# Performance work log

Hardware: AMD Instinct MI355X
Metric: run time of the kernel (lower is better)

Reference implementation:

```python
import jax, jax.numpy as jnp
import numpy as np

B, C, H, W = 64, 32, 112, 112
RANK = 3


def setup_inputs() -> dict:
    key = jax.random.key(0)
    k1, k2, k3, k4, k5 = jax.random.split(key, 5)
    N = H * W  # 12544
    return {
        "x": jax.random.uniform(k1, (B, C, H, W), dtype=jnp.float32),
        "p_buffer": jax.random.normal(k2, (B, N, RANK), dtype=jnp.float32),
        "q_buffer": jax.random.normal(k3, (B, C, RANK), dtype=jnp.float32),
        "grad_p_buffer": jax.random.normal(k4, (B, N, RANK), dtype=jnp.float32),
        "grad_q_buffer": jax.random.normal(k5, (B, C, RANK), dtype=jnp.float32),
        "n_iter": 2,
    }


def _power_svd(X, P, Q, n_iter):
    # X: [b, c, n]; P: [b, n, r]; Q: [b, c, r]
    for i in range(n_iter):
        if i == n_iter - 1:
            P = jnp.linalg.qr(P)[0]  # batched reduced QR, tall-skinny (n x r)
        Q = jnp.einsum('bcn,bnr->bcr', X, P)
        if i == n_iter - 1:
            Q = jnp.linalg.qr(Q)[0]  # batched reduced QR (c x r)
        P = jnp.einsum('bcn,bcr->bnr', X, Q)  # X^T @ Q
    return P, Q


def reference(x, p_buffer, q_buffer, grad_p_buffer, grad_q_buffer, n_iter):
    shape = x.shape
    X = x.reshape(shape[0], shape[1], -1)  # [B, C, H*W]
    P, Q = _power_svd(X, p_buffer, q_buffer, n_iter)
    # low-rank reconstruction Q @ P^T, back to original shape
    return jnp.einsum('bcr,bnr->bcn', Q, P).reshape(shape)
```

## Files before the change

### kernel.cpp

```cpp
#include <hip/hip_runtime.h>
#include <math.h>

#define N_HW 12544
#define TN 128
#define NCH 98
#define KB 16

#define WS_QG 65536
#define WS_U  (WS_QG + 64*96)
#define ZTOT  (WS_U)

typedef __attribute__((ext_vector_type(8)))  short short8;
typedef __attribute__((ext_vector_type(16))) float f32x16;
typedef __attribute__((ext_vector_type(4)))  float f32x4;

#define MFMA(a, b, c) __builtin_amdgcn_mfma_f32_32x32x16_bf16((a), (b), (c), 0, 0, 0)

__device__ __forceinline__ void split3(float f, ushort& h, ushort& m, ushort& l) {
    unsigned u = __builtin_bit_cast(unsigned, f);
    h = (ushort)(u >> 16);
    float fh = __builtin_bit_cast(float, u & 0xffff0000u);
    float rm = f - fh;
    unsigned um = __builtin_bit_cast(unsigned, rm);
    m = (ushort)(um >> 16);
    float fm = __builtin_bit_cast(float, um & 0xffff0000u);
    float rl = rm - fm;
    l = (ushort)(__builtin_bit_cast(unsigned, rl) >> 16);
}

__device__ __forceinline__ int xq(int c, int o) {
    return c * 16 + ((o & 8) | ((o ^ c) & 7));
}

__global__ __launch_bounds__(256)
void k0_zero(float* __restrict__ ws)
{
    const int g = blockIdx.x * 256 + threadIdx.x;
    if (g < ZTOT / 4) ((float4*)ws)[g] = make_float4(0.f, 0.f, 0.f, 0.f);
}

__global__ __launch_bounds__(256)
void k1_gram(const float* __restrict__ x, const float* __restrict__ p,
             float* __restrict__ Sg, float* __restrict__ Qg)
{
    const int b = blockIdx.y, kb = blockIdx.x;
    const int tid = threadIdx.x;
    const int lane = tid & 63, wave = tid >> 6;

    __shared__ uint4 XS[3 * 512];
    __shared__ alignas(16) ushort PTH[3 * TN], PTM[3 * TN], PTL[3 * TN];
    __shared__ float Ssum[1024], T2[1024], T3[1024];
    float* dmp = (float*)XS;

    const int c = tid >> 3, oc = tid & 7;
    const float* xrow = x + ((size_t)b * 32 + c) * N_HW;
    const float* pbat = p + (size_t)b * N_HW * 3;

    f32x16 D1 = {0,0,0,0,0,0,0,0,0,0,0,0,0,0,0,0};
    f32x16 D2 = {0,0,0,0,0,0,0,0,0,0,0,0,0,0,0,0};
    f32x16 D3 = {0,0,0,0,0,0,0,0,0,0,0,0,0,0,0,0};
    f32x16 DQ = {0,0,0,0,0,0,0,0,0,0,0,0,0,0,0,0};
    const int cl = lane & 31, g = lane >> 5;
    const int rr = (cl < 3) ? cl : 0;

    float4 pre[4];
    float prep[3];
    int j = kb;
    {
        const float4* xr = (const float4*)(xrow + (size_t)j * TN);
        pre[0] = xr[2 * oc];      pre[1] = xr[2 * oc + 1];
        pre[2] = xr[2 * oc + 16]; pre[3] = xr[2 * oc + 17];
        if (tid < TN) {
            const float* pb = pbat + (size_t)(j * TN + tid) * 3;
            prep[0] = pb[0]; prep[1] = pb[1]; prep[2] = pb[2];
        }
    }

    while (true) {
        #pragma unroll
        for (int t = 0; t < 2; ++t) {
            const int o = oc + 8 * t;
            float4 f0 = pre[2 * t], f1 = pre[2 * t + 1];
            float fv[8] = {f0.x, f0.y, f0.z, f0.w, f1.x, f1.y, f1.z, f1.w};
            unsigned hw[4], mw[4], lw[4];
            #pragma unroll
            for (int i = 0; i < 4; ++i) {
                ushort h0, m0, l0, h1, m1, l1;
                split3(fv[2 * i],     h0, m0, l0);
                split3(fv[2 * i + 1], h1, m1, l1);
                hw[i] = (unsigned)h0 | ((unsigned)h1 << 16);
                mw[i] = (unsigned)m0 | ((unsigned)m1 << 16);
                lw[i] = (unsigned)l0 | ((unsigned)l1 << 16);
            }
            const int s = xq(c, o);
            XS[s]        = make_uint4(hw[0], hw[1], hw[2], hw[3]);
            XS[512 + s]  = make_uint4(mw[0], mw[1], mw[2], mw[3]);
            XS[1024 + s] = make_uint4(lw[0], lw[1], lw[2], lw[3]);
        }
        if (tid < TN) {
            #pragma unroll
            for (int r = 0; r < 3; ++r) {
                ushort h, m, l;
                split3(prep[r], h, m, l);
                PTH[r * TN + tid] = h; PTM[r * TN + tid] = m; PTL[r * TN + tid] = l;
            }
        }

        const int jn = j + KB;
        const bool more = (jn < NCH);
        if (more) {
            const float4* xr = (const float4*)(xrow + (size_t)jn * TN);
            pre[0] = xr[2 * oc];      pre[1] = xr[2 * oc + 1];
            pre[2] = xr[2 * oc + 16]; pre[3] = xr[2 * oc + 17];
            if (tid < TN) {
                const float* pb = pbat + (size_t)(jn * TN + tid) * 3;
                prep[0] = pb[0]; prep[1] = pb[1]; prep[2] = pb[2];
            }
        }
        __syncthreads();

        for (int s = wave; s < 8; s += 4) {
            const int sl = xq(cl, 2 * s + g);
            short8 xh = __builtin_bit_cast(short8, XS[sl]);
            short8 xm = __builtin_bit_cast(short8, XS[512 + sl]);
            short8 xl = __builtin_bit_cast(short8, XS[1024 + sl]);
            const int po = rr * TN + 16 * s + 8 * g;
            short8 ph = *(const short8*)&PTH[po];
            short8 pm = *(const short8*)&PTM[po];
            short8 pl = *(const short8*)&PTL[po];
            D1 = MFMA(xh, xh, D1);
            D1 = MFMA(xm, xm, D1);
            D2 = MFMA(xh, xm, D2);
            D3 = MFMA(xh, xl, D3);
            DQ = MFMA(xh, ph, DQ);
            DQ = MFMA(xh, pm, DQ);
            DQ = MFMA(xm, ph, DQ);
            DQ = MFMA(xh, pl, DQ);
            DQ = MFMA(xl, ph, DQ);
            DQ = MFMA(xm, pm, DQ);
        }

        if (!more) break;
        j = jn;
        __syncthreads();
    }

    #define DUMP_REDUCE(D, dst)                                                            \
        __syncthreads();                                                                   \
        _Pragma("unroll")                                                                  \
        for (int i = 0; i < 4; ++i)                                                        \
            *(float4*)&dmp[tid * 20 + 4 * i] =                                             \
                make_float4((D)[4*i], (D)[4*i+1], (D)[4*i+2], (D)[4*i+3]);                 \
        __syncthreads();                                                                   \
        _Pragma("unroll")                                                                  \
        for (int it = 0; it < 4; ++it) {                                                   \
            const int e = tid + 256 * it;                                                  \
            const int r = e >> 5, co = e & 31;                                             \
            const int ln = co + 32 * ((r >> 2) & 1);                                       \
            const int rg = (r & 3) + 4 * (r >> 3);                                         \
            (dst)[e] = dmp[ln * 20 + rg] + dmp[(64 + ln) * 20 + rg]                        \
                     + dmp[(128 + ln) * 20 + rg] + dmp[(192 + ln) * 20 + rg];              \
        }

    DUMP_REDUCE(D1, Ssum)
    DUMP_REDUCE(D2, T2)
    DUMP_REDUCE(D3, T3)
    __syncthreads();
    {
        float* Sb = Sg + (size_t)b * 1024;
        #pragma unroll
        for (int it = 0; it < 4; ++it) {
            const int e = tid + 256 * it;
            const int r = e >> 5, co = e & 31;
            const int et = (co << 5) | r;
            atomicAdd(&Sb[e], Ssum[e] + T2[e] + T2[et] + T3[e] + T3[et]);
        }
    }
    __syncthreads();
    #pragma unroll
    for (int i = 0; i < 4; ++i)
        *(float4*)&dmp[tid * 20 + 4 * i] = make_float4(DQ[4*i], DQ[4*i+1], DQ[4*i+2], DQ[4*i+3]);
    __syncthreads();
    if (tid < 96) {
        const int c2 = tid / 3, r2 = tid - 3 * c2;
        const int ln = r2 + 32 * ((c2 >> 2) & 1);
        const int rg = (c2 & 3) + 4 * (c2 >> 3);
        float s = dmp[ln * 20 + rg] + dmp[(64 + ln) * 20 + rg]
                + dmp[(128 + ln) * 20 + rg] + dmp[(192 + ln) * 20 + rg];
        atomicAdd(&Qg[(size_t)b * 96 + tid], s);
    }
}

__global__ __launch_bounds__(128)
void k2_solve(const float* __restrict__ Sg, const float* __restrict__ Qg,
              float* __restrict__ Uo)
{
    const int b = blockIdx.x, tid = threadIdx.x;
    __shared__ float S[1024];
    __shared__ float Qv[96];
    __shared__ float V[96];
    __shared__ float G[6], L[6];

    #pragma unroll
    for (int i = 0; i < 8; ++i) S[tid + 128 * i] = Sg[(size_t)b * 1024 + tid + 128 * i];
    if (tid < 96) Qv[tid] = Qg[(size_t)b * 96 + tid];
    __syncthreads();
    if (tid < 96) {
        const int c = tid / 3, r = tid % 3;
        float s = 0.f;
        #pragma unroll 8
        for (int cc = 0; cc < 32; ++cc) s += S[c * 32 + cc] * Qv[cc * 3 + r];
        V[tid] = s;
    }
    for (int round = 0; round < 2; ++round) {
        __syncthreads();
        if (tid < 6) {
            const int r = (tid > 2) ? 2 : ((tid > 0) ? 1 : 0);
            const int s = tid - (r * (r + 1)) / 2;
            float g = 0.f;
            for (int c = 0; c < 32; ++c) g += V[c * 3 + r] * V[c * 3 + s];
            G[tid] = g;
        }
        __syncthreads();
        if (tid == 0) {
            const float l00 = sqrtf(G[0]);
            const float l10 = G[1] / l00, l20 = G[3] / l00;
            const float l11 = sqrtf(G[2] - l10 * l10);
            const float l21 = (G[4] - l20 * l10) / l11;
            const float l22 = sqrtf(G[5] - l20 * l20 - l21 * l21);
            L[0] = l00; L[1] = l10; L[2] = l11; L[3] = l20; L[4] = l21; L[5] = l22;
        }
        __syncthreads();
        if (tid < 32) {
            const float v0 = V[tid * 3 + 0], v1 = V[tid * 3 + 1], v2 = V[tid * 3 + 2];
            const float u0 = v0 / L[0];
            const float u1 = (v1 - L[1] * u0) / L[2];
            const float u2 = (v2 - L[3] * u0 - L[4] * u1) / L[5];
            V[tid * 3 + 0] = u0; V[tid * 3 + 1] = u1; V[tid * 3 + 2] = u2;
        }
    }
    __syncthreads();
    if (tid < 32) {
        Uo[(size_t)b * 128 + tid * 4 + 0] = V[tid * 3 + 0];
        Uo[(size_t)b * 128 + tid * 4 + 1] = V[tid * 3 + 1];
        Uo[(size_t)b * 128 + tid * 4 + 2] = V[tid * 3 + 2];
        Uo[(size_t)b * 128 + tid * 4 + 3] = 0.f;
    }
}

__global__ __launch_bounds__(256)
void k3_out(const float* __restrict__ x, const float* __restrict__ Uw,
            float* __restrict__ out)
{
    const int b = blockIdx.y, tid = threadIdx.x;
    __shared__ float Us[32][4];
    if (tid < 128) ((float*)Us)[tid] = Uw[(size_t)b * 128 + tid];
    __syncthreads();
    const int g = blockIdx.x * 256 + tid;
    if (g >= N_HW / 4) return;

    const float* Xb = x   + (size_t)b * 32 * N_HW + 4 * (size_t)g;
    float*       Ob = out + (size_t)b * 32 * N_HW + 4 * (size_t)g;

    float t0x = 0, t0y = 0, t0z = 0, t0w = 0;
    float t1x = 0, t1y = 0, t1z = 0, t1w = 0;
    float t2x = 0, t2y = 0, t2z = 0, t2w = 0;
    #pragma unroll 16
    for (int c = 0; c < 32; ++c) {
        float4 xv = *(const float4*)(Xb + (size_t)c * N_HW);
        const float u0 = Us[c][0], u1 = Us[c][1], u2 = Us[c][2];
        t0x += u0 * xv.x; t0y += u0 * xv.y; t0z += u0 * xv.z; t0w += u0 * xv.w;
        t1x += u1 * xv.x; t1y += u1 * xv.y; t1z += u1 * xv.z; t1w += u1 * xv.w;
        t2x += u2 * xv.x; t2y += u2 * xv.y; t2z += u2 * xv.z; t2w += u2 * xv.w;
    }
    #pragma unroll 16
    for (int c = 0; c < 32; ++c) {
        const float u0 = Us[c][0], u1 = Us[c][1], u2 = Us[c][2];
        f32x4 o;
        o.x = u0 * t0x + u1 * t1x + u2 * t2x;
        o.y = u0 * t0y + u1 * t1y + u2 * t2y;
        o.z = u0 * t0z + u1 * t1z + u2 * t2z;
        o.w = u0 * t0w + u1 * t1w + u2 * t2w;
        __builtin_nontemporal_store(o, (f32x4*)(Ob + (size_t)c * N_HW));
    }
}

extern "C" void kernel_launch(void* const* d_in, const int* in_sizes, int n_in,
                              void* d_out, int out_size, void* d_ws, size_t ws_size,
                              hipStream_t stream)
{
    const float* x = (const float*)d_in[0];
    const float* p = (const float*)d_in[1];
    float* ws = (float*)d_ws;
    float* Sg = ws;
    float* Qg = ws + WS_QG;
    float* U  = ws + WS_U;
    float* out = (float*)d_out;

    hipLaunchKernelGGL(k0_zero, dim3((ZTOT / 4 + 255) / 256), dim3(256), 0, stream, ws);
    hipLaunchKernelGGL(k1_gram, dim3(KB, 64), dim3(256), 0, stream, x, p, Sg, Qg);
    hipLaunchKernelGGL(k2_solve, dim3(64), dim3(128), 0, stream, Sg, Qg, U);
    hipLaunchKernelGGL(k3_out, dim3((N_HW / 4 + 255) / 256, 64), dim3(256), 0, stream, x, U, out);
}
```

Baseline: 232.5 us.

## Replace atomic gram accumulation with per-block partials reduced in solve kernel

Each gram block now writes its partial Gram and Q sums to its own workspace slot, and the solve kernel sums them, instead of zeroing the workspace and reducing with global atomics. This removes the zeroing launch and the atomic traffic. The D3 accumulator is merged into D2, so one fewer LDS dump/reduce is needed. The grid split goes from 16 to 24 blocks per batch for more parallelism, at the cost of more partial data for the solve kernel to read serially.

```diff
diff --git a/kernel.cpp b/kernel.cpp
--- a/kernel.cpp
+++ b/kernel.cpp
@@ -4,11 +4,12 @@
 #define N_HW 12544
 #define TN 128
 #define NCH 98
-#define KB 16
-
-#define WS_QG 65536
-#define WS_U  (WS_QG + 64*96)
-#define ZTOT  (WS_U)
+#define KB 24
+
+#define WS_P1 0
+#define WS_P2 (64 * KB * 1024)
+#define WS_QP (2 * 64 * KB * 1024)
+#define WS_U  (WS_QP + 64 * KB * 96)
 
 typedef __attribute__((ext_vector_type(8)))  short short8;
 typedef __attribute__((ext_vector_type(16))) float f32x16;
@@ -33,15 +34,8 @@
 }
 
 __global__ __launch_bounds__(256)
-void k0_zero(float* __restrict__ ws)
-{
-    const int g = blockIdx.x * 256 + threadIdx.x;
-    if (g < ZTOT / 4) ((float4*)ws)[g] = make_float4(0.f, 0.f, 0.f, 0.f);
-}
-
-__global__ __launch_bounds__(256)
 void k1_gram(const float* __restrict__ x, const float* __restrict__ p,
-             float* __restrict__ Sg, float* __restrict__ Qg)
+             float* __restrict__ P1, float* __restrict__ P2, float* __restrict__ Qp)
 {
     const int b = blockIdx.y, kb = blockIdx.x;
     const int tid = threadIdx.x;
@@ -49,7 +43,6 @@
 
     __shared__ uint4 XS[3 * 512];
     __shared__ alignas(16) ushort PTH[3 * TN], PTM[3 * TN], PTL[3 * TN];
-    __shared__ float Ssum[1024], T2[1024], T3[1024];
     float* dmp = (float*)XS;
 
     const int c = tid >> 3, oc = tid & 7;
@@ -58,7 +51,6 @@
 
     f32x16 D1 = {0,0,0,0,0,0,0,0,0,0,0,0,0,0,0,0};
     f32x16 D2 = {0,0,0,0,0,0,0,0,0,0,0,0,0,0,0,0};
-    f32x16 D3 = {0,0,0,0,0,0,0,0,0,0,0,0,0,0,0,0};
     f32x16 DQ = {0,0,0,0,0,0,0,0,0,0,0,0,0,0,0,0};
     const int cl = lane & 31, g = lane >> 5;
     const int rr = (cl < 3) ? cl : 0;
@@ -131,7 +123,7 @@
             D1 = MFMA(xh, xh, D1);
             D1 = MFMA(xm, xm, D1);
             D2 = MFMA(xh, xm, D2);
-            D3 = MFMA(xh, xl, D3);
+            D2 = MFMA(xh, xl, D2);
             DQ = MFMA(xh, ph, DQ);
             DQ = MFMA(xh, pm, DQ);
             DQ = MFMA(xm, ph, DQ);
@@ -145,7 +137,7 @@
         __syncthreads();
     }
 
-    #define DUMP_REDUCE(D, dst)                                                            \
+    #define DUMP_REDUCE_G(D, gdst)                                                         \
         __syncthreads();                                                                   \
         _Pragma("unroll")                                                                  \
         for (int i = 0; i < 4; ++i)                                                        \
@@ -158,24 +150,15 @@
             const int r = e >> 5, co = e & 31;                                             \
             const int ln = co + 32 * ((r >> 2) & 1);                                       \
             const int rg = (r & 3) + 4 * (r >> 3);                                         \
-            (dst)[e] = dmp[ln * 20 + rg] + dmp[(64 + ln) * 20 + rg]                        \
-                     + dmp[(128 + ln) * 20 + rg] + dmp[(192 + ln) * 20 + rg];              \
-        }
-
-    DUMP_REDUCE(D1, Ssum)
-    DUMP_REDUCE(D2, T2)
-    DUMP_REDUCE(D3, T3)
-    __syncthreads();
-    {
-        float* Sb = Sg + (size_t)b * 1024;
-        #pragma unroll
-        for (int it = 0; it < 4; ++it) {
-            const int e = tid + 256 * it;
-            const int r = e >> 5, co = e & 31;
-            const int et = (co << 5) | r;
-            atomicAdd(&Sb[e], Ssum[e] + T2[e] + T2[et] + T3[e] + T3[et]);
-        }
-    }
+            (gdst)[e] = dmp[ln * 20 + rg] + dmp[(64 + ln) * 20 + rg]                       \
+                      + dmp[(128 + ln) * 20 + rg] + dmp[(192 + ln) * 20 + rg];             \
+        }
+
+    float* p1 = P1 + ((size_t)b * KB + kb) * 1024;
+    float* p2 = P2 + ((size_t)b * KB + kb) * 1024;
+    DUMP_REDUCE_G(D1, p1)
+    DUMP_REDUCE_G(D2, p2)
+
     __syncthreads();
     #pragma unroll
     for (int i = 0; i < 4; ++i)
@@ -187,24 +170,45 @@
         const int rg = (c2 & 3) + 4 * (c2 >> 3);
         float s = dmp[ln * 20 + rg] + dmp[(64 + ln) * 20 + rg]
                 + dmp[(128 + ln) * 20 + rg] + dmp[(192 + ln) * 20 + rg];
-        atomicAdd(&Qg[(size_t)b * 96 + tid], s);
-    }
-}
-
-__global__ __launch_bounds__(128)
-void k2_solve(const float* __restrict__ Sg, const float* __restrict__ Qg,
-              float* __restrict__ Uo)
+        Qp[((size_t)b * KB + kb) * 96 + tid] = s;
+    }
+}
+
+__global__ __launch_bounds__(256)
+void k2_solve(const float* __restrict__ P1, const float* __restrict__ P2,
+              const float* __restrict__ Qp, float* __restrict__ Uo)
 {
     const int b = blockIdx.x, tid = threadIdx.x;
-    __shared__ float S[1024];
-    __shared__ float Qv[96];
-    __shared__ float V[96];
-    __shared__ float G[6], L[6];
-
+    __shared__ float S[1024], A2[1024];
+    __shared__ float Qv[96], V[96], G[6], L[6];
+
+    float a1[4] = {0.f, 0.f, 0.f, 0.f}, a2[4] = {0.f, 0.f, 0.f, 0.f};
+    const float* p1 = P1 + (size_t)b * KB * 1024;
+    const float* p2 = P2 + (size_t)b * KB * 1024;
+    for (int kb = 0; kb < KB; ++kb) {
+        #pragma unroll
+        for (int i = 0; i < 4; ++i) {
+            a1[i] += p1[kb * 1024 + tid + 256 * i];
+            a2[i] += p2[kb * 1024 + tid + 256 * i];
+        }
+    }
     #pragma unroll
-    for (int i = 0; i < 8; ++i) S[tid + 128 * i] = Sg[(size_t)b * 1024 + tid + 128 * i];
-    if (tid < 96) Qv[tid] = Qg[(size_t)b * 96 + tid];
-    __syncthreads();
+    for (int i = 0; i < 4; ++i) A2[tid + 256 * i] = a2[i];
+    if (tid < 96) {
+        const float* qp = Qp + (size_t)b * KB * 96;
+        float q = 0.f;
+        for (int kb = 0; kb < KB; ++kb) q += qp[kb * 96 + tid];
+        Qv[tid] = q;
+    }
+    __syncthreads();
+    #pragma unroll
+    for (int i = 0; i < 4; ++i) {
+        const int e = tid + 256 * i;
+        const int et = ((e & 31) << 5) | (e >> 5);
+        S[e] = a1[i] + a2[i] + A2[et];
+    }
+    __syncthreads();
+
     if (tid < 96) {
         const int c = tid / 3, r = tid % 3;
         float s = 0.f;
@@ -292,13 +296,13 @@
     const float* x = (const float*)d_in[0];
     const float* p = (const float*)d_in[1];
     float* ws = (float*)d_ws;
-    float* Sg = ws;
-    float* Qg = ws + WS_QG;
+    float* P1 = ws + WS_P1;
+    float* P2 = ws + WS_P2;
+    float* Qp = ws + WS_QP;
     float* U  = ws + WS_U;
     float* out = (float*)d_out;
 
-    hipLaunchKernelGGL(k0_zero, dim3((ZTOT / 4 + 255) / 256), dim3(256), 0, stream, ws);
-    hipLaunchKernelGGL(k1_gram, dim3(KB, 64), dim3(256), 0, stream, x, p, Sg, Qg);
-    hipLaunchKernelGGL(k2_solve, dim3(64), dim3(128), 0, stream, Sg, Qg, U);
+    hipLaunchKernelGGL(k1_gram, dim3(KB, 64), dim3(256), 0, stream, x, p, P1, P2, Qp);
+    hipLaunchKernelGGL(k2_solve, dim3(64), dim3(256), 0, stream, P1, P2, Qp, U);
     hipLaunchKernelGGL(k3_out, dim3((N_HW / 4 + 255) / 256, 64), dim3(256), 0, stream, x, U, out);
 }
```

After: 231.8 us. Within noise of the previous version (-0.3%).
